# Performance work log

Measured on AMD Instinct MI355X. Metric: run time of the kernel, lower is better.

## Reference

```python
import jax, jax.numpy as jnp
import numpy as np

B, C, T, V, H = 128, 128, 64, 25, 4
EPS = 1e-5


def _bn(x, g, b, m, v):
    # eval-mode BatchNorm2d over channel axis 1 of [B,C,T,V]
    inv = g / jnp.sqrt(v + EPS)
    return x * inv[:, None, None] + (b - m * inv)[:, None, None]


def setup_inputs() -> dict:
    key = jax.random.key(0)
    ks = jax.random.split(key, 12)
    s = 0.05
    return {
        "x": jax.random.normal(ks[0], (B, C, T, V), jnp.float32),
        "bn0_gamma": jnp.ones((C,), jnp.float32),
        "bn0_beta": jnp.zeros((C,), jnp.float32),
        "bn0_mean": jax.random.normal(ks[1], (C,), jnp.float32) * s,
        "bn0_var": jnp.abs(jax.random.normal(ks[2], (C,), jnp.float32)) + 1.0,
        "conv1_w": jax.random.normal(ks[3], (2 * C, C), jnp.float32) * (1.0 / np.sqrt(C)),
        "conv1_b": jax.random.normal(ks[4], (2 * C,), jnp.float32) * s,
        "bn1_gamma": jnp.ones((C,), jnp.float32),
        "bn1_beta": jnp.zeros((C,), jnp.float32),
        "bn1_mean": jax.random.normal(ks[5], (C,), jnp.float32) * s,
        "bn1_var": jnp.abs(jax.random.normal(ks[6], (C,), jnp.float32)) + 1.0,
        "bn2_gamma": jnp.ones((C,), jnp.float32),
        "bn2_beta": jnp.zeros((C,), jnp.float32),
        "bn2_mean": jax.random.normal(ks[7], (C,), jnp.float32) * s,
        "bn2_var": jnp.abs(jax.random.normal(ks[8], (C,), jnp.float32)) + 1.0,
        "shared_topology": jnp.tile(jnp.eye(V, dtype=jnp.float32)[None], (H, 1, 1))
                           + jax.random.normal(ks[9], (H, V, V), jnp.float32) * s,
        "spatial_weight": jax.random.normal(ks[10], (H, V, V), jnp.float32) * s,
        "conv2_w": jax.random.normal(ks[11], (C, C), jnp.float32) * (1.0 / np.sqrt(C)),
        "conv2_b": jnp.zeros((C,), jnp.float32),
    }


def reference(x, bn0_gamma, bn0_beta, bn0_mean, bn0_var,
              conv1_w, conv1_b,
              bn1_gamma, bn1_beta, bn1_mean, bn1_var,
              bn2_gamma, bn2_beta, bn2_mean, bn2_var,
              shared_topology, spatial_weight,
              conv2_w, conv2_b):
    residual = x
    h = _bn(x, bn0_gamma, bn0_beta, bn0_mean, bn0_var)
    # conv1: 1x1 conv C -> 2C
    h = jnp.einsum('oc,bctv->botv', conv1_w, h) + conv1_b[None, :, None, None]
    h = jax.nn.gelu(h, approximate=False)  # torch nn.GELU default is exact
    z1, z2 = jnp.split(h, 2, axis=1)
    z1 = _bn(z1, bn1_gamma, bn1_beta, bn1_mean, bn1_var)
    z2 = _bn(z2, bn2_gamma, bn2_beta, bn2_mean, bn2_var)
    D = C // H
    z1 = z1.reshape(B, H, D, T, V)
    z2 = z2.reshape(B, H, D, T, V)
    y1 = jnp.einsum('huv,bhdtv->bhdtu', shared_topology, z1)
    attn = jnp.einsum('huv,bhdtv->bhdtu', spatial_weight, z2)
    y = (y1 + z1 * attn).reshape(B, C, T, V)
    y = jnp.einsum('oc,bctv->botv', conv2_w, y) + conv2_b[None, :, None, None]
    return jax.nn.relu(y + residual)
```

## Files before the change

kernel.cpp:

```cpp
#include <hip/hip_runtime.h>
#include <math.h>

#define C_   128
#define T_   64
#define V_   25
#define TV   1600
#define CTV  204800
#define EPS  1e-5f
#define TT   2
#define NC   64
#define HS   136
#define ZS   72

typedef __bf16 bf16x8 __attribute__((ext_vector_type(8)));
typedef float  f32x4  __attribute__((ext_vector_type(4)));

__device__ __forceinline__ float gelu_exact(float x) {
  float y = fabsf(x) * 0.70710678118654752440f;
  float t = __builtin_amdgcn_rcpf(fmaf(0.3275911f, y, 1.0f));
  float p = fmaf(1.061405429f, t, -1.453152027f);
  p = fmaf(p, t, 1.421413741f);
  p = fmaf(p, t, -0.284496736f);
  p = fmaf(p, t, 0.254829592f);
  p = p * t;
  float s = p * __expf(-y * y);
  float hxs = 0.5f * x * s;
  return x >= 0.0f ? x - hxs : hxs;
}

__global__ __launch_bounds__(256) void prep_pack(
    const float* __restrict__ W1, const float* __restrict__ W2,
    const float* __restrict__ topo, const float* __restrict__ spat,
    __bf16* __restrict__ W1p, __bf16* __restrict__ W2p, __bf16* __restrict__ Sp) {
  int i = blockIdx.x * 256 + threadIdx.x;
  if (i < 32768) {
    int j = i & 7, l = (i >> 3) & 63, ks = (i >> 9) & 3, mt = i >> 11;
    int o = mt * 16 + (l & 15);
    int c = ks * 32 + ((l >> 4) << 3) + j;
    W1p[i] = (__bf16)W1[o * 128 + c];
  }
  if (i < 16384) {
    int j = i & 7, l = (i >> 3) & 63, ks = (i >> 9) & 3, mt = i >> 11;
    int o = mt * 16 + (l & 15);
    int c = ks * 32 + ((l >> 4) << 3) + j;
    W2p[i] = (__bf16)W2[o * 128 + c];
  }
  if (i < 8192) {
    int j = i & 7, l = (i >> 3) & 63, mt = (i >> 9) & 1, mat = (i >> 10) & 1, h = i >> 11;
    int u = mt * 16 + (l & 15);
    int v = ((l >> 4) << 3) + j;
    const float* src = mat ? spat : topo;
    Sp[i] = (__bf16)((u < 25 && v < 25) ? src[h * 625 + u * 25 + v] : 0.0f);
  }
}

__global__ __launch_bounds__(512, 4) void fused_v4(
    const float* __restrict__ x,
    const float* __restrict__ bn0g, const float* __restrict__ bn0b,
    const float* __restrict__ bn0m, const float* __restrict__ bn0v,
    const float* __restrict__ b1,
    const float* __restrict__ bn1g, const float* __restrict__ bn1b,
    const float* __restrict__ bn1m, const float* __restrict__ bn1v,
    const float* __restrict__ bn2g, const float* __restrict__ bn2b,
    const float* __restrict__ bn2m, const float* __restrict__ bn2v,
    const float* __restrict__ b2,
    const __bf16* __restrict__ W1p, const __bf16* __restrict__ W2p,
    const __bf16* __restrict__ Sp,
    float* __restrict__ out) {
  __shared__ __bf16 sM[NC * HS];
  __shared__ __bf16 sZ1[C_ * ZS];
  __shared__ __bf16 sZ2[C_ * ZS];
  __shared__ float  sInv[256], sAdd[256];
  __shared__ float  sB1[256], sB2[128];

  const int bt = blockIdx.x;
  const int b  = bt >> 5;
  const int tb = bt & 31;
  const float* xb = x   + (size_t)b * CTV + tb * (TT * V_);
  float*       ob = out + (size_t)b * CTV + tb * (TT * V_);
  const int tid  = threadIdx.x;
  const int wave = tid >> 6, lane = tid & 63;
  const int lr = lane & 15, lg = lane >> 4;

  const int h2 = wave >> 1, ch = wave & 1;
  bf16x8 at[2], as2[2];
  #pragma unroll
  for (int mt = 0; mt < 2; ++mt) {
    at[mt]  = *reinterpret_cast<const bf16x8*>(Sp + (((h2 * 2 + 0) * 2 + mt) << 9) + lane * 8);
    as2[mt] = *reinterpret_cast<const bf16x8*>(Sp + (((h2 * 2 + 1) * 2 + mt) << 9) + lane * 8);
  }

  if (tid < 256) {
    int o = tid;
    float g, bb, m, vv;
    if (o < 128) { g = bn1g[o]; bb = bn1b[o]; m = bn1m[o]; vv = bn1v[o]; }
    else { int c = o - 128; g = bn2g[c]; bb = bn2b[c]; m = bn2m[c]; vv = bn2v[c]; }
    float inv = g * rsqrtf(vv + EPS);
    sInv[o] = inv;
    sAdd[o] = fmaf(-m, inv, bb);
    sB1[o] = b1[o];
    if (o < 128) sB2[o] = b2[o];
  }
  {
    int buf = tid >> 8, c = (tid >> 1) & 127, t = tid & 1;
    bf16x8 zz = {};
    *reinterpret_cast<bf16x8*>((buf ? sZ2 : sZ1) + c * ZS + t * 32 + 24) = zz;
  }
  {
    const int c = tid >> 2, q = tid & 3;
    const int t = q & 1, vh = q >> 1;
    const int v0 = vh ? 13 : 0, v1 = vh ? 25 : 13;
    float inv = bn0g[c] * rsqrtf(bn0v[c] + EPS);
    float add = fmaf(-bn0m[c], inv, bn0b[c]);
    const float* xr = xb + c * TV + t * V_;
    for (int v = v0; v < v1; ++v)
      sM[(t * 32 + v) * HS + c] = (__bf16)fmaf(xr[v], inv, add);
  }
  __syncthreads();

  {
    f32x4 acc[2][4] = {};
    #pragma unroll
    for (int ks = 0; ks < 4; ++ks) {
      bf16x8 af[2];
      #pragma unroll
      for (int m2 = 0; m2 < 2; ++m2)
        af[m2] = *reinterpret_cast<const bf16x8*>(W1p + (((wave * 2 + m2) * 4 + ks) << 9) + lane * 8);
      bf16x8 bfr[4];
      #pragma unroll
      for (int n4 = 0; n4 < 4; ++n4)
        bfr[n4] = *reinterpret_cast<const bf16x8*>(&sM[(n4 * 16 + lr) * HS + ks * 32 + lg * 8]);
      #pragma unroll
      for (int m2 = 0; m2 < 2; ++m2)
        #pragma unroll
        for (int n4 = 0; n4 < 4; ++n4)
          acc[m2][n4] = __builtin_amdgcn_mfma_f32_16x16x32_bf16(af[m2], bfr[n4], acc[m2][n4], 0, 0, 0);
    }
    #pragma unroll
    for (int n4 = 0; n4 < 4; ++n4) {
      const int col = n4 * 16 + lr;
      const int v = col & 31;
      if (v < V_) {
        #pragma unroll
        for (int m2 = 0; m2 < 2; ++m2) {
          const int obase = (wave * 2 + m2) * 16 + lg * 4;
          #pragma unroll
          for (int r = 0; r < 4; ++r) {
            const int o = obase + r;
            float a = acc[m2][n4][r] + sB1[o];
            float z = fmaf(gelu_exact(a), sInv[o], sAdd[o]);
            if (o < 128) sZ1[o * ZS + col]         = (__bf16)z;
            else         sZ2[(o - 128) * ZS + col] = (__bf16)z;
          }
        }
      }
    }
  }
  __syncthreads();

  {
    const int cbase = h2 * 32 + ch * 16;
    f32x4 accY[2][2] = {}, accA[2][2] = {};
    #pragma unroll
    for (int t = 0; t < 2; ++t) {
      bf16x8 bz1 = *reinterpret_cast<const bf16x8*>(&sZ1[(cbase + lr) * ZS + t * 32 + lg * 8]);
      bf16x8 bz2 = *reinterpret_cast<const bf16x8*>(&sZ2[(cbase + lr) * ZS + t * 32 + lg * 8]);
      #pragma unroll
      for (int mt = 0; mt < 2; ++mt) {
        accY[mt][t] = __builtin_amdgcn_mfma_f32_16x16x32_bf16(at[mt],  bz1, accY[mt][t], 0, 0, 0);
        accA[mt][t] = __builtin_amdgcn_mfma_f32_16x16x32_bf16(as2[mt], bz2, accA[mt][t], 0, 0, 0);
      }
    }
    const int c = cbase + lr;
    #pragma unroll
    for (int mt = 0; mt < 2; ++mt) {
      #pragma unroll
      for (int t = 0; t < 2; ++t) {
        #pragma unroll
        for (int r = 0; r < 4; ++r) {
          const int u = mt * 16 + lg * 4 + r;
          if (u < V_) {
            float z1u = (float)sZ1[c * ZS + t * 32 + u];
            float yv = fmaf(z1u, accA[mt][t][r], accY[mt][t][r]);
            sM[(t * 32 + u) * HS + c] = (__bf16)yv;
          }
        }
      }
    }
  }
  __syncthreads();

  {
    f32x4 acc[4] = {};
    #pragma unroll
    for (int ks = 0; ks < 4; ++ks) {
      bf16x8 af = *reinterpret_cast<const bf16x8*>(W2p + ((wave * 4 + ks) << 9) + lane * 8);
      #pragma unroll
      for (int n4 = 0; n4 < 4; ++n4) {
        bf16x8 bfr = *reinterpret_cast<const bf16x8*>(&sM[(n4 * 16 + lr) * HS + ks * 32 + lg * 8]);
        acc[n4] = __builtin_amdgcn_mfma_f32_16x16x32_bf16(af, bfr, acc[n4], 0, 0, 0);
      }
    }
    #pragma unroll
    for (int n4 = 0; n4 < 4; ++n4) {
      const int col = n4 * 16 + lr;
      const int u = col & 31, t = col >> 5;
      if (u < V_) {
        #pragma unroll
        for (int r = 0; r < 4; ++r) {
          const int o = wave * 16 + lg * 4 + r;
          const int off = o * TV + t * V_ + u;
          float val = acc[n4][r] + sB2[o] + xb[off];
          ob[off] = fmaxf(val, 0.0f);
        }
      }
    }
  }
}

extern "C" void kernel_launch(void* const* d_in, const int* in_sizes, int n_in,
                              void* d_out, int out_size, void* d_ws, size_t ws_size,
                              hipStream_t stream) {
  const float* x    = (const float*)d_in[0];
  const float* bn0g = (const float*)d_in[1];
  const float* bn0b = (const float*)d_in[2];
  const float* bn0m = (const float*)d_in[3];
  const float* bn0v = (const float*)d_in[4];
  const float* W1   = (const float*)d_in[5];
  const float* b1   = (const float*)d_in[6];
  const float* bn1g = (const float*)d_in[7];
  const float* bn1b = (const float*)d_in[8];
  const float* bn1m = (const float*)d_in[9];
  const float* bn1v = (const float*)d_in[10];
  const float* bn2g = (const float*)d_in[11];
  const float* bn2b = (const float*)d_in[12];
  const float* bn2m = (const float*)d_in[13];
  const float* bn2v = (const float*)d_in[14];
  const float* topo = (const float*)d_in[15];
  const float* spat = (const float*)d_in[16];
  const float* W2   = (const float*)d_in[17];
  const float* b2   = (const float*)d_in[18];
  float* out = (float*)d_out;

  __bf16* W1p = (__bf16*)d_ws;
  __bf16* W2p = W1p + 32768;
  __bf16* Sp  = W2p + 16384;

  prep_pack<<<128, 256, 0, stream>>>(W1, W2, topo, spat, W1p, W2p, Sp);
  fused_v4<<<4096, 512, 0, stream>>>(
      x, bn0g, bn0b, bn0m, bn0v, b1,
      bn1g, bn1b, bn1m, bn1v, bn2g, bn2b, bn2m, bn2v,
      b2, W1p, W2p, Sp, out);
}
```

Measured before the change: 115.5 us.

## Fold BN0 into conv1 weights and alias LDS buffers for higher occupancy

The input BatchNorm is folded into the packed conv1 weights and a precomputed bias (extra prep block), so the main kernel stages raw x into shared memory. Shared memory is cut from three buffers to two aliased buffers (sA/sB), with extra barriers and re-zeroing of padding rows so regions can be reused across stages. Launch bounds go from 4 to 8 blocks per CU to raise occupancy. In exchange it adds syncs and register-held intermediates (yv), which raise register pressure under the tighter bound and may cause spills.

```diff
diff --git a/kernel.cpp b/kernel.cpp
--- a/kernel.cpp
+++ b/kernel.cpp
@@ -8,7 +8,6 @@
 #define CTV  204800
 #define EPS  1e-5f
 #define TT   2
-#define NC   64
 #define HS   136
 #define ZS   72
 
@@ -31,13 +30,29 @@
 __global__ __launch_bounds__(256) void prep_pack(
     const float* __restrict__ W1, const float* __restrict__ W2,
     const float* __restrict__ topo, const float* __restrict__ spat,
-    __bf16* __restrict__ W1p, __bf16* __restrict__ W2p, __bf16* __restrict__ Sp) {
+    const float* __restrict__ b1,
+    const float* __restrict__ bn0g, const float* __restrict__ bn0b,
+    const float* __restrict__ bn0m, const float* __restrict__ bn0v,
+    __bf16* __restrict__ W1p, __bf16* __restrict__ W2p, __bf16* __restrict__ Sp,
+    float* __restrict__ b1a) {
+  if (blockIdx.x == 128) {
+    int o = threadIdx.x;
+    float acc = b1[o];
+    for (int c = 0; c < 128; ++c) {
+      float inv = bn0g[c] * rsqrtf(bn0v[c] + EPS);
+      float add = fmaf(-bn0m[c], inv, bn0b[c]);
+      acc = fmaf(W1[o * 128 + c], add, acc);
+    }
+    b1a[o] = acc;
+    return;
+  }
   int i = blockIdx.x * 256 + threadIdx.x;
   if (i < 32768) {
     int j = i & 7, l = (i >> 3) & 63, ks = (i >> 9) & 3, mt = i >> 11;
     int o = mt * 16 + (l & 15);
     int c = ks * 32 + ((l >> 4) << 3) + j;
-    W1p[i] = (__bf16)W1[o * 128 + c];
+    float inv = bn0g[c] * rsqrtf(bn0v[c] + EPS);
+    W1p[i] = (__bf16)(W1[o * 128 + c] * inv);
   }
   if (i < 16384) {
     int j = i & 7, l = (i >> 3) & 63, ks = (i >> 9) & 3, mt = i >> 11;
@@ -54,24 +69,19 @@
   }
 }
 
-__global__ __launch_bounds__(512, 4) void fused_v4(
+__global__ __launch_bounds__(512, 8) void fused_v5(
     const float* __restrict__ x,
-    const float* __restrict__ bn0g, const float* __restrict__ bn0b,
-    const float* __restrict__ bn0m, const float* __restrict__ bn0v,
-    const float* __restrict__ b1,
     const float* __restrict__ bn1g, const float* __restrict__ bn1b,
     const float* __restrict__ bn1m, const float* __restrict__ bn1v,
     const float* __restrict__ bn2g, const float* __restrict__ bn2b,
     const float* __restrict__ bn2m, const float* __restrict__ bn2v,
     const float* __restrict__ b2,
     const __bf16* __restrict__ W1p, const __bf16* __restrict__ W2p,
-    const __bf16* __restrict__ Sp,
+    const __bf16* __restrict__ Sp,  const float* __restrict__ b1a,
     float* __restrict__ out) {
-  __shared__ __bf16 sM[NC * HS];
-  __shared__ __bf16 sZ1[C_ * ZS];
-  __shared__ __bf16 sZ2[C_ * ZS];
-  __shared__ float  sInv[256], sAdd[256];
-  __shared__ float  sB1[256], sB2[128];
+  __shared__ __bf16 sA[9216];
+  __shared__ __bf16 sB[9216];
+  __shared__ float  sInv[256], sAdd[256], sB1a[256], sB2[128];
 
   const int bt = blockIdx.x;
   const int b  = bt >> 5;
@@ -82,14 +92,6 @@
   const int wave = tid >> 6, lane = tid & 63;
   const int lr = lane & 15, lg = lane >> 4;
 
-  const int h2 = wave >> 1, ch = wave & 1;
-  bf16x8 at[2], as2[2];
-  #pragma unroll
-  for (int mt = 0; mt < 2; ++mt) {
-    at[mt]  = *reinterpret_cast<const bf16x8*>(Sp + (((h2 * 2 + 0) * 2 + mt) << 9) + lane * 8);
-    as2[mt] = *reinterpret_cast<const bf16x8*>(Sp + (((h2 * 2 + 1) * 2 + mt) << 9) + lane * 8);
-  }
-
   if (tid < 256) {
     int o = tid;
     float g, bb, m, vv;
@@ -98,28 +100,32 @@
     float inv = g * rsqrtf(vv + EPS);
     sInv[o] = inv;
     sAdd[o] = fmaf(-m, inv, bb);
-    sB1[o] = b1[o];
+    sB1a[o] = b1a[o];
     if (o < 128) sB2[o] = b2[o];
   }
-  {
-    int buf = tid >> 8, c = (tid >> 1) & 127, t = tid & 1;
+  for (int i = tid; i < 238; i += 512) {
+    int rowIdx = i / 17, k = i - rowIdx * 17;
+    int row = (rowIdx < 7 ? 25 + rowIdx : 50 + rowIdx);
     bf16x8 zz = {};
-    *reinterpret_cast<bf16x8*>((buf ? sZ2 : sZ1) + c * ZS + t * 32 + 24) = zz;
+    *reinterpret_cast<bf16x8*>(sA + row * HS + k * 8) = zz;
+  }
+  if (tid < 256) {
+    int c = tid >> 1, t = tid & 1;
+    bf16x8 zz = {};
+    *reinterpret_cast<bf16x8*>(sB + c * ZS + t * 32 + 24) = zz;
   }
   {
     const int c = tid >> 2, q = tid & 3;
     const int t = q & 1, vh = q >> 1;
     const int v0 = vh ? 13 : 0, v1 = vh ? 25 : 13;
-    float inv = bn0g[c] * rsqrtf(bn0v[c] + EPS);
-    float add = fmaf(-bn0m[c], inv, bn0b[c]);
     const float* xr = xb + c * TV + t * V_;
     for (int v = v0; v < v1; ++v)
-      sM[(t * 32 + v) * HS + c] = (__bf16)fmaf(xr[v], inv, add);
-  }
-  __syncthreads();
-
-  {
-    f32x4 acc[2][4] = {};
+      sA[(t * 32 + v) * HS + c] = (__bf16)xr[v];
+  }
+  __syncthreads();
+
+  f32x4 acc[2][4] = {};
+  {
     #pragma unroll
     for (int ks = 0; ks < 4; ++ks) {
       bf16x8 af[2];
@@ -129,13 +135,24 @@
       bf16x8 bfr[4];
       #pragma unroll
       for (int n4 = 0; n4 < 4; ++n4)
-        bfr[n4] = *reinterpret_cast<const bf16x8*>(&sM[(n4 * 16 + lr) * HS + ks * 32 + lg * 8]);
+        bfr[n4] = *reinterpret_cast<const bf16x8*>(&sA[(n4 * 16 + lr) * HS + ks * 32 + lg * 8]);
       #pragma unroll
       for (int m2 = 0; m2 < 2; ++m2)
         #pragma unroll
         for (int n4 = 0; n4 < 4; ++n4)
           acc[m2][n4] = __builtin_amdgcn_mfma_f32_16x16x32_bf16(af[m2], bfr[n4], acc[m2][n4], 0, 0, 0);
     }
+  }
+  __syncthreads();
+
+  {
+    if (tid < 256) {
+      int c = tid >> 1, t = tid & 1;
+      #pragma unroll
+      for (int pv = 25; pv < 32; ++pv)
+        sA[c * ZS + t * 32 + pv] = (__bf16)0.0f;
+    }
+    __bf16* zdst = (wave < 4) ? sB : sA;
     #pragma unroll
     for (int n4 = 0; n4 < 4; ++n4) {
       const int col = n4 * 16 + lr;
@@ -147,10 +164,9 @@
           #pragma unroll
           for (int r = 0; r < 4; ++r) {
             const int o = obase + r;
-            float a = acc[m2][n4][r] + sB1[o];
+            float a = acc[m2][n4][r] + sB1a[o];
             float z = fmaf(gelu_exact(a), sInv[o], sAdd[o]);
-            if (o < 128) sZ1[o * ZS + col]         = (__bf16)z;
-            else         sZ2[(o - 128) * ZS + col] = (__bf16)z;
+            zdst[(o & 127) * ZS + col] = (__bf16)z;
           }
         }
       }
@@ -158,13 +174,21 @@
   }
   __syncthreads();
 
-  {
-    const int cbase = h2 * 32 + ch * 16;
+  float yv[2][2][4];
+  const int h2 = wave >> 1, ch = wave & 1;
+  const int cbase = h2 * 32 + ch * 16;
+  {
+    bf16x8 at[2], as2[2];
+    #pragma unroll
+    for (int mt = 0; mt < 2; ++mt) {
+      at[mt]  = *reinterpret_cast<const bf16x8*>(Sp + (((h2 * 2 + 0) * 2 + mt) << 9) + lane * 8);
+      as2[mt] = *reinterpret_cast<const bf16x8*>(Sp + (((h2 * 2 + 1) * 2 + mt) << 9) + lane * 8);
+    }
     f32x4 accY[2][2] = {}, accA[2][2] = {};
     #pragma unroll
     for (int t = 0; t < 2; ++t) {
-      bf16x8 bz1 = *reinterpret_cast<const bf16x8*>(&sZ1[(cbase + lr) * ZS + t * 32 + lg * 8]);
-      bf16x8 bz2 = *reinterpret_cast<const bf16x8*>(&sZ2[(cbase + lr) * ZS + t * 32 + lg * 8]);
+      bf16x8 bz1 = *reinterpret_cast<const bf16x8*>(&sB[(cbase + lr) * ZS + t * 32 + lg * 8]);
+      bf16x8 bz2 = *reinterpret_cast<const bf16x8*>(&sA[(cbase + lr) * ZS + t * 32 + lg * 8]);
       #pragma unroll
       for (int mt = 0; mt < 2; ++mt) {
         accY[mt][t] = __builtin_amdgcn_mfma_f32_16x16x32_bf16(at[mt],  bz1, accY[mt][t], 0, 0, 0);
@@ -173,32 +197,47 @@
     }
     const int c = cbase + lr;
     #pragma unroll
-    for (int mt = 0; mt < 2; ++mt) {
-      #pragma unroll
-      for (int t = 0; t < 2; ++t) {
+    for (int mt = 0; mt < 2; ++mt)
+      #pragma unroll
+      for (int t = 0; t < 2; ++t)
         #pragma unroll
         for (int r = 0; r < 4; ++r) {
           const int u = mt * 16 + lg * 4 + r;
-          if (u < V_) {
-            float z1u = (float)sZ1[c * ZS + t * 32 + u];
-            float yv = fmaf(z1u, accA[mt][t][r], accY[mt][t][r]);
-            sM[(t * 32 + u) * HS + c] = (__bf16)yv;
-          }
-        }
-      }
-    }
-  }
-  __syncthreads();
-
-  {
-    f32x4 acc[4] = {};
+          float z1u = (u < V_) ? (float)sB[c * ZS + t * 32 + u] : 0.0f;
+          yv[mt][t][r] = fmaf(z1u, accA[mt][t][r], accY[mt][t][r]);
+        }
+  }
+  __syncthreads();
+
+  {
+    for (int i = tid; i < 238; i += 512) {
+      int rowIdx = i / 17, k = i - rowIdx * 17;
+      int row = (rowIdx < 7 ? 25 + rowIdx : 50 + rowIdx);
+      bf16x8 zz = {};
+      *reinterpret_cast<bf16x8*>(sB + row * HS + k * 8) = zz;
+    }
+    const int c = cbase + lr;
+    #pragma unroll
+    for (int mt = 0; mt < 2; ++mt)
+      #pragma unroll
+      for (int t = 0; t < 2; ++t)
+        #pragma unroll
+        for (int r = 0; r < 4; ++r) {
+          const int u = mt * 16 + lg * 4 + r;
+          if (u < V_) sB[(t * 32 + u) * HS + c] = (__bf16)yv[mt][t][r];
+        }
+  }
+  __syncthreads();
+
+  {
+    f32x4 acc2[4] = {};
     #pragma unroll
     for (int ks = 0; ks < 4; ++ks) {
       bf16x8 af = *reinterpret_cast<const bf16x8*>(W2p + ((wave * 4 + ks) << 9) + lane * 8);
       #pragma unroll
       for (int n4 = 0; n4 < 4; ++n4) {
-        bf16x8 bfr = *reinterpret_cast<const bf16x8*>(&sM[(n4 * 16 + lr) * HS + ks * 32 + lg * 8]);
-        acc[n4] = __builtin_amdgcn_mfma_f32_16x16x32_bf16(af, bfr, acc[n4], 0, 0, 0);
+        bf16x8 bfr = *reinterpret_cast<const bf16x8*>(&sB[(n4 * 16 + lr) * HS + ks * 32 + lg * 8]);
+        acc2[n4] = __builtin_amdgcn_mfma_f32_16x16x32_bf16(af, bfr, acc2[n4], 0, 0, 0);
       }
     }
     #pragma unroll
@@ -210,7 +249,7 @@
         for (int r = 0; r < 4; ++r) {
           const int o = wave * 16 + lg * 4 + r;
           const int off = o * TV + t * V_ + u;
-          float val = acc[n4][r] + sB2[o] + xb[off];
+          float val = acc2[n4][r] + sB2[o] + xb[off];
           ob[off] = fmaxf(val, 0.0f);
         }
       }
@@ -245,10 +284,12 @@
   __bf16* W1p = (__bf16*)d_ws;
   __bf16* W2p = W1p + 32768;
   __bf16* Sp  = W2p + 16384;
-
-  prep_pack<<<128, 256, 0, stream>>>(W1, W2, topo, spat, W1p, W2p, Sp);
-  fused_v4<<<4096, 512, 0, stream>>>(
-      x, bn0g, bn0b, bn0m, bn0v, b1,
-      bn1g, bn1b, bn1m, bn1v, bn2g, bn2b, bn2m, bn2v,
-      b2, W1p, W2p, Sp, out);
-}
+  float*  b1a = (float*)((char*)d_ws + 114688);
+
+  prep_pack<<<129, 256, 0, stream>>>(W1, W2, topo, spat, b1,
+                                     bn0g, bn0b, bn0m, bn0v,
+                                     W1p, W2p, Sp, b1a);
+  fused_v5<<<4096, 512, 0, stream>>>(
+      x, bn1g, bn1b, bn1m, bn1v, bn2g, bn2b, bn2m, bn2v,
+      b2, W1p, W2p, Sp, b1a, out);
+}
```

After: 126.7 us. 9.7% more time.
